# Kernel tuning notes

Hardware: AMD Instinct MI355X
Metric: run time of the kernel (lower is better)

## Reference

```python
import jax, jax.numpy as jnp
import numpy as np

VOCAB = 50257
SEQ = 2048  # == max_sentence_size; positional add requires seq == max_sentence_size
DIM = 768
BATCH = 8


def setup_inputs() -> dict:
    key = jax.random.key(0)
    k1, k2, k3 = jax.random.split(key, 3)
    tokens = jax.random.randint(k1, (BATCH, SEQ), 0, VOCAB, dtype=jnp.int32)
    # nn.Linear(vocab, d).weight has shape [d, vocab]
    W_emb = jax.random.normal(k2, (DIM, VOCAB), dtype=jnp.float32) * 0.02
    # nn.Linear(d, max_sentence).weight has shape [max_sentence, d]
    W_pos = jax.random.normal(k3, (SEQ, DIM), dtype=jnp.float32) * 0.02
    return {"tokens": tokens, "W_emb": W_emb, "W_pos": W_pos}


def reference(tokens, W_emb, W_pos):
    # Original: one_hot(tokens, vocab) @ W_emb.T  -- mathematically a gather
    # of rows of W_emb.T (= columns of W_emb). Expressed as an efficient take.
    tok_emb = jnp.take(W_emb.T, tokens, axis=0)  # (B, S, D)
    # Positional embedding broadcasts over batch: (S, D)
    return tok_emb + W_pos
```

## Files before the change

kernel.cpp:

```cpp
#include <hip/hip_runtime.h>

#define BATCH 8
#define SEQ   2048
#define DIM   768
#define VOCAB 50257
#define NTOK  (BATCH * SEQ)
#define NBUCKET 3142
#define SORT_THREADS 1024

typedef float f32x4 __attribute__((ext_vector_type(4)));

__global__ __launch_bounds__(SORT_THREADS) void sort_tokens_kernel(
    const int* __restrict__ tokens, unsigned* __restrict__ ws)
{
    __shared__ unsigned cnt[4096];
    __shared__ unsigned wsum[16];
    const int tid = threadIdx.x;

    for (int j = tid; j < 4096; j += SORT_THREADS) cnt[j] = 0;
    __syncthreads();

    for (int i = tid; i < NTOK; i += SORT_THREADS) {
        int t = tokens[i];
        atomicAdd(&cnt[t >> 4], 1u);
    }
    __syncthreads();

    unsigned c0 = cnt[4*tid+0], c1 = cnt[4*tid+1], c2 = cnt[4*tid+2], c3 = cnt[4*tid+3];
    unsigned tsum = c0 + c1 + c2 + c3;
    unsigned x = tsum;
    for (int off = 1; off < 64; off <<= 1) {
        unsigned y = __shfl_up(x, off, 64);
        if ((tid & 63) >= off) x += y;
    }
    if ((tid & 63) == 63) wsum[tid >> 6] = x;
    __syncthreads();
    if (tid < 16) {
        unsigned w = wsum[tid];
        for (int off = 1; off < 16; off <<= 1) {
            unsigned y = __shfl_up(w, off, 64);
            if (tid >= off) w += y;
        }
        wsum[tid] = w;
    }
    __syncthreads();
    unsigned wavebase = (tid >= 64) ? wsum[(tid >> 6) - 1] : 0u;
    unsigned excl = wavebase + x - tsum;
    cnt[4*tid+0] = excl;
    cnt[4*tid+1] = excl + c0;
    cnt[4*tid+2] = excl + c0 + c1;
    cnt[4*tid+3] = excl + c0 + c1 + c2;
    __syncthreads();

    for (int i = tid; i < NTOK; i += SORT_THREADS) {
        int t = tokens[i];
        unsigned p = atomicAdd(&cnt[t >> 4], 1u);
        ws[p] = ((unsigned)t << 14) | (unsigned)i;
    }
}

__global__ __launch_bounds__(192) void emb_pos_kernel(
    const unsigned* __restrict__ ws,
    const float*    __restrict__ W_emb,
    const float*    __restrict__ W_pos,
    float*          __restrict__ out)
{
    const int bid  = blockIdx.x;
    const int sidx = ((bid & 7) << 11) | (bid >> 3);
    const unsigned packed = ws[sidx];
    const int t = (int)(packed >> 14);
    const int i = (int)(packed & 16383u);
    const int s = i & (SEQ - 1);

    const int d = threadIdx.x * 4;

    const float* we = W_emb + (size_t)d * VOCAB + t;
    const f32x4 p  = *reinterpret_cast<const f32x4*>(W_pos + s * DIM + d);

    f32x4 r;
    r.x = we[0]                 + p.x;
    r.y = we[(size_t)VOCAB]     + p.y;
    r.z = we[(size_t)2 * VOCAB] + p.z;
    r.w = we[(size_t)3 * VOCAB] + p.w;

    __builtin_nontemporal_store(r, reinterpret_cast<f32x4*>(out + (size_t)i * DIM + d));
}

extern "C" void kernel_launch(void* const* d_in, const int* in_sizes, int n_in,
                              void* d_out, int out_size, void* d_ws, size_t ws_size,
                              hipStream_t stream) {
    const int*   tokens = (const int*)  d_in[0];
    const float* W_emb  = (const float*)d_in[1];
    const float* W_pos  = (const float*)d_in[2];
    float*       out    = (float*)d_out;
    unsigned*    ws     = (unsigned*)d_ws;

    sort_tokens_kernel<<<dim3(1), dim3(SORT_THREADS), 0, stream>>>(tokens, ws);
    emb_pos_kernel<<<dim3(NTOK), dim3(192), 0, stream>>>(ws, W_emb, W_pos, out);
}
```

Before: 294.8 us.

## Gather embeddings per 16-token vocab bucket via an LDS-transposed slab

The sort kernel now also writes the per-bucket start offsets to the workspace. The per-token gather kernel is replaced by one block per 16-wide vocab bucket. Each block loads a 16x768 slab of W_emb with vector loads, transposes it into shared memory, then serves every sorted token in that bucket: it adds the positional row and does a non-temporal store of the output row. This replaces the scattered 4-byte column reads that each token made with wider loads shared across the bucket. The cost is about 49KB of LDS per block, which limits occupancy, a serial per-bucket token loop, and vector loads from rows whose stride is not a multiple of four floats, so many of them are unaligned.

```diff
diff --git a/kernel.cpp b/kernel.cpp
--- a/kernel.cpp
+++ b/kernel.cpp
@@ -6,7 +6,9 @@
 #define VOCAB 50257
 #define NTOK  (BATCH * SEQ)
 #define NBUCKET 3142
+#define OFF_BASE NTOK
 #define SORT_THREADS 1024
+#define LDS_PITCH 772
 
 typedef float f32x4 __attribute__((ext_vector_type(4)));
 
@@ -52,6 +54,9 @@
     cnt[4*tid+3] = excl + c0 + c1 + c2;
     __syncthreads();
 
+    for (int j = tid; j < 4096; j += SORT_THREADS) ws[OFF_BASE + j] = cnt[j];
+    __syncthreads();
+
     for (int i = tid; i < NTOK; i += SORT_THREADS) {
         int t = tokens[i];
         unsigned p = atomicAdd(&cnt[t >> 4], 1u);
@@ -59,31 +64,56 @@
     }
 }
 
-__global__ __launch_bounds__(192) void emb_pos_kernel(
+__global__ __launch_bounds__(256) void emb_slab_kernel(
     const unsigned* __restrict__ ws,
     const float*    __restrict__ W_emb,
     const float*    __restrict__ W_pos,
     float*          __restrict__ out)
 {
-    const int bid  = blockIdx.x;
-    const int sidx = ((bid & 7) << 11) | (bid >> 3);
-    const unsigned packed = ws[sidx];
-    const int t = (int)(packed >> 14);
-    const int i = (int)(packed & 16383u);
-    const int s = i & (SEQ - 1);
+    __shared__ float slab[16 * LDS_PITCH];
 
-    const int d = threadIdx.x * 4;
+    const int c = blockIdx.x;
+    const unsigned start = ws[OFF_BASE + c];
+    const unsigned end   = ws[OFF_BASE + c + 1];
+    if (start == end) return;
 
-    const float* we = W_emb + (size_t)d * VOCAB + t;
-    const f32x4 p  = *reinterpret_cast<const f32x4*>(W_pos + s * DIM + d);
+    const int base = (16 * c <= VOCAB - 16) ? 16 * c : (VOCAB - 16);
 
-    f32x4 r;
-    r.x = we[0]                 + p.x;
-    r.y = we[(size_t)VOCAB]     + p.y;
-    r.z = we[(size_t)2 * VOCAB] + p.z;
-    r.w = we[(size_t)3 * VOCAB] + p.w;
+    const int tid = threadIdx.x;
+    const int q  = tid & 3;
+    const int r0 = tid >> 2;
 
-    __builtin_nontemporal_store(r, reinterpret_cast<f32x4*>(out + (size_t)i * DIM + d));
+    f32x4 v[12];
+    #pragma unroll
+    for (int it = 0; it < 12; ++it) {
+        const int r = r0 + it * 64;
+        v[it] = *reinterpret_cast<const f32x4*>(W_emb + (size_t)r * VOCAB + base + 4 * q);
+    }
+    #pragma unroll
+    for (int it = 0; it < 12; ++it) {
+        const int r = r0 + it * 64;
+        slab[(4*q + 0) * LDS_PITCH + r] = v[it].x;
+        slab[(4*q + 1) * LDS_PITCH + r] = v[it].y;
+        slab[(4*q + 2) * LDS_PITCH + r] = v[it].z;
+        slab[(4*q + 3) * LDS_PITCH + r] = v[it].w;
+    }
+    __syncthreads();
+
+    if (tid < 192) {
+        const int d4 = tid * 4;
+        for (unsigned idx = start; idx < end; ++idx) {
+            const unsigned packed = ws[idx];
+            const int t = (int)(packed >> 14);
+            const int i = (int)(packed & 16383u);
+            const int s = i & (SEQ - 1);
+            const int j = t - base;
+
+            const f32x4 col = *reinterpret_cast<const f32x4*>(&slab[j * LDS_PITCH + d4]);
+            const f32x4 p   = *reinterpret_cast<const f32x4*>(W_pos + s * DIM + d4);
+            const f32x4 rr  = col + p;
+            __builtin_nontemporal_store(rr, reinterpret_cast<f32x4*>(out + (size_t)i * DIM + d4));
+        }
+    }
 }
 
 extern "C" void kernel_launch(void* const* d_in, const int* in_sizes, int n_in,
@@ -96,5 +126,5 @@
     unsigned*    ws     = (unsigned*)d_ws;
 
     sort_tokens_kernel<<<dim3(1), dim3(SORT_THREADS), 0, stream>>>(tokens, ws);
-    emb_pos_kernel<<<dim3(NTOK), dim3(192), 0, stream>>>(ws, W_emb, W_pos, out);
+    emb_slab_kernel<<<dim3(NBUCKET), dim3(256), 0, stream>>>(ws, W_emb, W_pos, out);
 }
```

Measured after the change: 270.6 us. -8.2%, faster.
